# Performance work log

Hardware: AMD Instinct MI355X
Metric: run time of the kernel (lower is better)

## Reference

```python
import jax, jax.numpy as jnp
import numpy as np

N, IN_DIM, H, D = 4096, 512, 4, 64


def setup_inputs() -> dict:
    key = jax.random.key(0)
    k1, k2, k3, k4 = jax.random.split(key, 4)
    features = jax.random.normal(k1, (N, IN_DIM), dtype=jnp.float32)
    adjacency = jax.random.randint(k2, (N, N), 0, 2, dtype=jnp.int32)
    weights = jax.random.normal(k3, (IN_DIM, D * H), dtype=jnp.float32) * (1.414 / np.sqrt(IN_DIM))
    attention = jax.random.normal(k4, (1, H, 2 * D), dtype=jnp.float32) * 0.1
    bias = jnp.zeros((D * H,), dtype=jnp.float32)
    return {"features": features, "adjacency": adjacency, "weights": weights,
            "attention": attention, "bias": bias}


def reference(features, adjacency, weights, attention, bias):
    n = features.shape[0]
    h = (features @ weights).reshape(n, H, D)  # [N, H, D]
    # e[i,j,h] = leakyrelu(a1_h . h_i + a2_h . h_j)  (concat-attention decomposed)
    a1 = attention[0, :, :D]   # [H, D]
    a2 = attention[0, :, D:]   # [H, D]
    s1 = jnp.einsum('nhd,hd->nh', h, a1)  # [N, H]
    s2 = jnp.einsum('nhd,hd->nh', h, a2)  # [N, H]
    e = jax.nn.leaky_relu(s1[:, None, :] + s2[None, :, :], negative_slope=0.2)  # [N, N, H]
    masked = jnp.where(adjacency[:, :, None] > 0, e, jnp.float32(-9e15))
    attn = jax.nn.softmax(masked, axis=1)  # softmax over neighbors j (dim=1)
    out = jnp.einsum('ijh,jhd->ihd', attn, h).reshape(n, H * D)
    return out + bias
```

## Files before the change

### kernel.cpp

```cpp
#include <hip/hip_runtime.h>
#include <hip/hip_bf16.h>

#define N_NODES 4096
#define IN_DIMC 512
#define NHEADS 4
#define DHEAD 64
#define OUT_COLS 256
#define HPB (N_NODES * DHEAD * 2)

typedef __attribute__((ext_vector_type(8))) short short8;
typedef __attribute__((ext_vector_type(4))) float f32x4;

__device__ __forceinline__ short bf16b(float x) {
    return __builtin_bit_cast(short, __float2bfloat16(x));
}
__device__ __forceinline__ void gload16(const void* g, void* l) {
    __builtin_amdgcn_global_load_lds((const __attribute__((address_space(1))) void*)g,
                                     (__attribute__((address_space(3))) void*)l,
                                     16, 0, 0);
}
__device__ __forceinline__ void gload4(const void* g, void* l) {
    __builtin_amdgcn_global_load_lds((const __attribute__((address_space(1))) void*)g,
                                     (__attribute__((address_space(3))) void*)l,
                                     4, 0, 0);
}

__global__ __launch_bounds__(256) void k_prep2(
    const float* __restrict__ A, const float* __restrict__ W,
    const float* __restrict__ att, const int* __restrict__ adj,
    char* __restrict__ hP, float* __restrict__ E1, float* __restrict__ F1,
    float* __restrict__ E2, float* __restrict__ F2,
    unsigned long long* __restrict__ bitsT)
{
    const int t = (int)threadIdx.x;
    if (blockIdx.x >= 512) {
        const int pb = (int)blockIdx.x - 512;
        const int i = pb * 4 + (t >> 6);
        const int lane = t & 63;
        const int* arow = adj + (size_t)i * N_NODES;
        #pragma unroll 2
        for (int it = 0; it < 16; ++it) {
            const int c = it * 4;
            const int a0 = arow[(c + 0) * 64 + lane];
            const int a1 = arow[(c + 1) * 64 + lane];
            const int a2 = arow[(c + 2) * 64 + lane];
            const int a3 = arow[(c + 3) * 64 + lane];
            const unsigned long long m0 = __ballot(a0 != 0);
            const unsigned long long m1 = __ballot(a1 != 0);
            const unsigned long long m2 = __ballot(a2 != 0);
            const unsigned long long m3 = __ballot(a3 != 0);
            if (lane == 0) {
                bitsT[(size_t)(c + 0) * N_NODES + i] = m0;
                bitsT[(size_t)(c + 1) * N_NODES + i] = m1;
                bitsT[(size_t)(c + 2) * N_NODES + i] = m2;
                bitsT[(size_t)(c + 3) * N_NODES + i] = m3;
            }
        }
        return;
    }
    __shared__ float As[32][36];
    __shared__ float Bs[32][68];
    __shared__ float ht[64][33];
    const int m0 = ((int)blockIdx.x & 127) * 32;
    const int head = (int)blockIdx.x >> 7;
    const int n0 = head * 64;
    const int tm = t & 7, tn = t >> 3;
    float acc[4][2] = {};
    for (int k0 = 0; k0 < IN_DIMC; k0 += 32) {
        {
            const int r = t >> 3, kc = (t & 7) << 2;
            float4 v0 = *(const float4*)(A + (size_t)(m0 + r) * IN_DIMC + k0 + kc);
            As[kc + 0][r] = v0.x; As[kc + 1][r] = v0.y; As[kc + 2][r] = v0.z; As[kc + 3][r] = v0.w;
            const int rb = t >> 4, nc = (t & 15) << 2;
            float4 w0 = *(const float4*)(W + (size_t)(k0 + rb) * OUT_COLS + n0 + nc);
            float4 w1 = *(const float4*)(W + (size_t)(k0 + rb + 16) * OUT_COLS + n0 + nc);
            *(float4*)&Bs[rb][nc] = w0;
            *(float4*)&Bs[rb + 16][nc] = w1;
        }
        __syncthreads();
        #pragma unroll
        for (int kk = 0; kk < 32; ++kk) {
            const f32x4 a = *(const f32x4*)&As[kk][tm << 2];
            const float b0 = Bs[kk][tn * 2], b1 = Bs[kk][tn * 2 + 1];
            #pragma unroll
            for (int i = 0; i < 4; ++i) {
                acc[i][0] = fmaf(a[i], b0, acc[i][0]);
                acc[i][1] = fmaf(a[i], b1, acc[i][1]);
            }
        }
        __syncthreads();
    }
    #pragma unroll
    for (int i = 0; i < 4; ++i) {
        ht[tn * 2 + 0][(tm << 2) + i] = acc[i][0];
        ht[tn * 2 + 1][(tm << 2) + i] = acc[i][1];
    }
    __syncthreads();
    {
        const int d = t >> 2, qq = t & 3;
        short8 hv;
        #pragma unroll
        for (int k = 0; k < 8; ++k) hv[k] = bf16b(ht[d][qq * 8 + k]);
        const size_t off16 = ((size_t)(m0 >> 5) * 4 + (d >> 4)) * 64 + qq * 16 + (d & 15);
        *(short8*)(hP + (size_t)head * HPB + off16 * 16) = hv;
    }
    {
        const int r = t >> 3, part = t & 7;
        float p1 = 0.f, p2 = 0.f;
        #pragma unroll
        for (int dd = 0; dd < 8; ++dd) {
            const int d = part * 8 + dd;
            const float v = ht[d][r];
            p1 = fmaf(v, att[head * 128 + d], p1);
            p2 = fmaf(v, att[head * 128 + 64 + d], p2);
        }
        p1 += __shfl_xor(p1, 1); p1 += __shfl_xor(p1, 2); p1 += __shfl_xor(p1, 4);
        p2 += __shfl_xor(p2, 1); p2 += __shfl_xor(p2, 2); p2 += __shfl_xor(p2, 4);
        if (part == 0) {
            const int idx = head * N_NODES + m0 + r;
            E1[idx] = __expf(p1);
            F1[idx] = __expf(0.2f * p1);
            E2[idx] = __expf(p2);
            F2[idx] = __expf(0.2f * p2);
        }
    }
}

__global__ __launch_bounds__(512, 2) void k_gat(
    const unsigned long long* __restrict__ bitsT, const char* __restrict__ hP,
    const float* __restrict__ E1, const float* __restrict__ F1,
    const float* __restrict__ E2, const float* __restrict__ F2,
    float* __restrict__ pA, float* __restrict__ pB, float* __restrict__ pDen)
{
    __shared__ __align__(16) char stage[8 * 18432];
    const int i0 = (int)blockIdx.x * 32;
    const int by = (int)blockIdx.y;
    const int t = (int)threadIdx.x;
    const int w = t >> 6, lane = t & 63, il = lane & 15, q = lane >> 4;
    const int head = w & 3, jseg = w >> 2;
    const int jbase = by * 2048 + jseg * 1024;
    char* myst = stage + w * 18432;
    const char* hPh = hP + (size_t)head * HPB;
    const float* E2h = E2 + head * N_NODES;
    const float* F2h = F2 + head * N_NODES;
    const float e1a = E1[head * N_NODES + i0 + il];
    const float e1b = E1[head * N_NODES + i0 + 16 + il];
    const float f1a = F1[head * N_NODES + i0 + il];
    const float f1b = F1[head * N_NODES + i0 + 16 + il];
    f32x4 acc[4][2] = {};
    f32x4 accD[2] = {};
    short8 ones;
    #pragma unroll
    for (int e = 0; e < 8; ++e) ones[e] = (short)0x3F80;

    const int g0 = jbase >> 5;
    const int c0 = jbase >> 6;
    auto issue = [&](int bs, char* dst) {
        const char* hsrc = hPh + (size_t)(g0 + bs * 2) * 4096;
        #pragma unroll
        for (int k = 0; k < 8; ++k)
            gload16(hsrc + k * 1024 + lane * 16, dst + k * 1024);
        gload4(E2h + jbase + bs * 64 + lane, dst + 8192);
        gload4(F2h + jbase + bs * 64 + lane, dst + 8448);
        gload4((const char*)(bitsT + (size_t)(c0 + bs) * N_NODES + i0) + lane * 4,
               dst + 8704);
    };
    issue(0, myst);
    #pragma unroll 2
    for (int s = 0; s < 16; ++s) {
        const int bs = (s + 1 < 16) ? s + 1 : 15;
        issue(bs, myst + ((s + 1) & 1) * 9216);
        asm volatile("s_waitcnt vmcnt(11)" ::: "memory");
        const char* base = myst + (s & 1) * 9216;
        const unsigned long long bitsA = *(const unsigned long long*)(base + 8704 + il * 8);
        const unsigned long long bitsB = *(const unsigned long long*)(base + 8704 + 128 + il * 8);
        #pragma unroll
        for (int h = 0; h < 2; ++h) {
            const f32x4 ea = *(const f32x4*)(base + 8192 + h * 128 + q * 32);
            const f32x4 eb = *(const f32x4*)(base + 8192 + h * 128 + q * 32 + 16);
            const f32x4 fa = *(const f32x4*)(base + 8448 + h * 128 + q * 32);
            const f32x4 fb2 = *(const f32x4*)(base + 8448 + h * 128 + q * 32 + 16);
            const unsigned mA = (unsigned)(bitsA >> (h * 32 + q * 8)) & 0xffu;
            const unsigned mB = (unsigned)(bitsB >> (h * 32 + q * 8)) & 0xffu;
            short8 afA, afB;
            #pragma unroll
            for (int e = 0; e < 8; ++e) {
                const float Ev = (e < 4) ? ea[e] : eb[e - 4];
                const float Fv = (e < 4) ? fa[e] : fb2[e - 4];
                const float pa = fmaxf(e1a * Ev, f1a * Fv);
                const float pb = fmaxf(e1b * Ev, f1b * Fv);
                afA[e] = bf16b(((mA >> e) & 1u) ? pa : 0.f);
                afB[e] = bf16b(((mB >> e) & 1u) ? pb : 0.f);
            }
            #pragma unroll
            for (int dblk = 0; dblk < 4; ++dblk) {
                const short8 bfrag = *(const short8*)(base + h * 4096 + dblk * 1024 + lane * 16);
                acc[dblk][0] = __builtin_amdgcn_mfma_f32_16x16x32_bf16(afA, bfrag, acc[dblk][0], 0, 0, 0);
                acc[dblk][1] = __builtin_amdgcn_mfma_f32_16x16x32_bf16(afB, bfrag, acc[dblk][1], 0, 0, 0);
            }
            accD[0] = __builtin_amdgcn_mfma_f32_16x16x32_bf16(afA, ones, accD[0], 0, 0, 0);
            accD[1] = __builtin_amdgcn_mfma_f32_16x16x32_bf16(afB, ones, accD[1], 0, 0, 0);
        }
    }
    __syncthreads();
    float* ep = (float*)stage;
    if (jseg == 1) {
        float* dst = ep + (w - 4) * 2560;
        #pragma unroll
        for (int dblk = 0; dblk < 4; ++dblk)
            #pragma unroll
            for (int sub = 0; sub < 2; ++sub)
                #pragma unroll
                for (int r = 0; r < 4; ++r)
                    dst[(dblk * 8 + sub * 4 + r) * 64 + lane] = acc[dblk][sub][r];
        #pragma unroll
        for (int sub = 0; sub < 2; ++sub)
            #pragma unroll
            for (int r = 0; r < 4; ++r)
                dst[(32 + sub * 4 + r) * 64 + lane] = accD[sub][r];
    }
    __syncthreads();
    if (jseg == 0) {
        const float* src = ep + w * 2560;
        float* po = (by == 0) ? pA : pB;
        #pragma unroll
        for (int sub = 0; sub < 2; ++sub) {
            #pragma unroll
            for (int r = 0; r < 4; ++r) {
                const int row = i0 + sub * 16 + q * 4 + r;
                #pragma unroll
                for (int dblk = 0; dblk < 4; ++dblk) {
                    const float v = acc[dblk][sub][r] + src[(dblk * 8 + sub * 4 + r) * 64 + lane];
                    po[(size_t)row * OUT_COLS + head * DHEAD + dblk * 16 + il] = v;
                }
                if (il == 0) {
                    const float d = accD[sub][r] + src[(32 + sub * 4 + r) * 64 + lane];
                    pDen[by * (NHEADS * N_NODES) + head * N_NODES + row] = d;
                }
            }
        }
    }
}

__global__ __launch_bounds__(256) void k_fin(
    const float* __restrict__ pB, const float* __restrict__ pDen,
    const float* __restrict__ bias, float* __restrict__ outp)
{
    const int gid = (int)blockIdx.x * 256 + (int)threadIdx.x;
    const int i = gid >> 6;
    const int c4 = (gid & 63) << 2;
    const int head = c4 >> 6;
    const float4 v0 = *(const float4*)(outp + (size_t)i * OUT_COLS + c4);
    const float4 v1 = *(const float4*)(pB + (size_t)i * OUT_COLS + c4);
    const float d = pDen[head * N_NODES + i] + pDen[NHEADS * N_NODES + head * N_NODES + i];
    const float inv = 1.0f / d;
    const float4 bb = *(const float4*)(bias + c4);
    float4 r;
    r.x = (v0.x + v1.x) * inv + bb.x;
    r.y = (v0.y + v1.y) * inv + bb.y;
    r.z = (v0.z + v1.z) * inv + bb.z;
    r.w = (v0.w + v1.w) * inv + bb.w;
    *(float4*)(outp + (size_t)i * OUT_COLS + c4) = r;
}

extern "C" void kernel_launch(void* const* d_in, const int* in_sizes, int n_in,
                              void* d_out, int out_size, void* d_ws, size_t ws_size,
                              hipStream_t stream) {
    const float* features  = (const float*)d_in[0];
    const int*   adjacency = (const int*)d_in[1];
    const float* weights   = (const float*)d_in[2];
    const float* attention = (const float*)d_in[3];
    const float* bias      = (const float*)d_in[4];
    float* out = (float*)d_out;

    char* ws = (char*)d_ws;
    char*  hP = ws;
    float* E1 = (float*)(ws + 2u*1024*1024);
    float* F1 = (float*)(ws + 2u*1024*1024 +  64u*1024);
    float* E2 = (float*)(ws + 2u*1024*1024 + 128u*1024);
    float* F2 = (float*)(ws + 2u*1024*1024 + 192u*1024);
    unsigned long long* bitsT =
        (unsigned long long*)(ws + 2u*1024*1024 + 256u*1024);
    float* pB   = (float*)(ws + 4u*1024*1024 + 256u*1024);
    float* pDen = (float*)(ws + 8u*1024*1024 + 256u*1024);

    k_prep2<<<dim3(1536), 256, 0, stream>>>(features, weights, attention, adjacency,
                                            hP, E1, F1, E2, F2, bitsT);
    k_gat<<<dim3(128, 2), 512, 0, stream>>>(bitsT, hP, E1, F1, E2, F2,
                                            out , pB, pDen);
    k_fin<<<dim3(1024), 256, 0, stream>>>(pB, pDen, bias, out);
}
```

Measured before the change: 58.75 us.

## Split GAT neighbor loop four ways with smaller 32-column stages

The attention-aggregation kernel now splits the neighbor dimension four ways instead of two, launching 512 blocks instead of 256. Each wave processes 32 neighbors per step with a halved LDS stage, and launch bounds are raised to four blocks per SM. The adjacency bitmask is stored as 32-bit words so each step can load only the bits it needs. The aim is more parallelism and occupancy on the main kernel, at the cost of two extra partial-output buffers that the final kernel must read and sum, and a shorter pipeline per block.

Measured after the change: 60.74 us. 3.4% more time.

```diff
diff --git a/kernel.cpp b/kernel.cpp
--- a/kernel.cpp
+++ b/kernel.cpp
@@ -30,7 +30,7 @@
     const float* __restrict__ att, const int* __restrict__ adj,
     char* __restrict__ hP, float* __restrict__ E1, float* __restrict__ F1,
     float* __restrict__ E2, float* __restrict__ F2,
-    unsigned long long* __restrict__ bitsT)
+    unsigned* __restrict__ bits32)
 {
     const int t = (int)threadIdx.x;
     if (blockIdx.x >= 512) {
@@ -50,10 +50,14 @@
             const unsigned long long m2 = __ballot(a2 != 0);
             const unsigned long long m3 = __ballot(a3 != 0);
             if (lane == 0) {
-                bitsT[(size_t)(c + 0) * N_NODES + i] = m0;
-                bitsT[(size_t)(c + 1) * N_NODES + i] = m1;
-                bitsT[(size_t)(c + 2) * N_NODES + i] = m2;
-                bitsT[(size_t)(c + 3) * N_NODES + i] = m3;
+                bits32[(size_t)(2 * c + 0) * N_NODES + i] = (unsigned)m0;
+                bits32[(size_t)(2 * c + 1) * N_NODES + i] = (unsigned)(m0 >> 32);
+                bits32[(size_t)(2 * c + 2) * N_NODES + i] = (unsigned)m1;
+                bits32[(size_t)(2 * c + 3) * N_NODES + i] = (unsigned)(m1 >> 32);
+                bits32[(size_t)(2 * c + 4) * N_NODES + i] = (unsigned)m2;
+                bits32[(size_t)(2 * c + 5) * N_NODES + i] = (unsigned)(m2 >> 32);
+                bits32[(size_t)(2 * c + 6) * N_NODES + i] = (unsigned)m3;
+                bits32[(size_t)(2 * c + 7) * N_NODES + i] = (unsigned)(m3 >> 32);
             }
         }
         return;
@@ -126,20 +130,21 @@
     }
 }
 
-__global__ __launch_bounds__(512, 2) void k_gat(
-    const unsigned long long* __restrict__ bitsT, const char* __restrict__ hP,
+__global__ __launch_bounds__(512, 4) void k_gat(
+    const unsigned* __restrict__ bits32, const char* __restrict__ hP,
     const float* __restrict__ E1, const float* __restrict__ F1,
     const float* __restrict__ E2, const float* __restrict__ F2,
-    float* __restrict__ pA, float* __restrict__ pB, float* __restrict__ pDen)
+    float* __restrict__ pA, float* __restrict__ pB,
+    float* __restrict__ pC, float* __restrict__ pD, float* __restrict__ pDen)
 {
-    __shared__ __align__(16) char stage[8 * 18432];
+    __shared__ __align__(16) char stage[8 * 9216];
     const int i0 = (int)blockIdx.x * 32;
     const int by = (int)blockIdx.y;
     const int t = (int)threadIdx.x;
     const int w = t >> 6, lane = t & 63, il = lane & 15, q = lane >> 4;
     const int head = w & 3, jseg = w >> 2;
-    const int jbase = by * 2048 + jseg * 1024;
-    char* myst = stage + w * 18432;
+    const int jbase = by * 1024 + jseg * 512;
+    char* myst = stage + w * 9216;
     const char* hPh = hP + (size_t)head * HPB;
     const float* E2h = E2 + head * N_NODES;
     const float* F2h = F2 + head * N_NODES;
@@ -154,53 +159,54 @@
     for (int e = 0; e < 8; ++e) ones[e] = (short)0x3F80;
 
     const int g0 = jbase >> 5;
-    const int c0 = jbase >> 6;
     auto issue = [&](int bs, char* dst) {
-        const char* hsrc = hPh + (size_t)(g0 + bs * 2) * 4096;
-        #pragma unroll
-        for (int k = 0; k < 8; ++k)
+        const char* hsrc = hPh + (size_t)(g0 + bs) * 4096;
+        #pragma unroll
+        for (int k = 0; k < 4; ++k)
             gload16(hsrc + k * 1024 + lane * 16, dst + k * 1024);
-        gload4(E2h + jbase + bs * 64 + lane, dst + 8192);
-        gload4(F2h + jbase + bs * 64 + lane, dst + 8448);
-        gload4((const char*)(bitsT + (size_t)(c0 + bs) * N_NODES + i0) + lane * 4,
-               dst + 8704);
+        if (lane < 32) {
+            gload4(E2h + jbase + bs * 32 + lane, dst + 4096);
+            gload4(F2h + jbase + bs * 32 + lane, dst + 4224);
+            gload4((const char*)(bits32 + (size_t)(g0 + bs) * N_NODES + i0) + lane * 4,
+                   dst + 4352);
+        }
     };
     issue(0, myst);
     #pragma unroll 2
     for (int s = 0; s < 16; ++s) {
-        const int bs = (s + 1 < 16) ? s + 1 : 15;
-        issue(bs, myst + ((s + 1) & 1) * 9216);
-        asm volatile("s_waitcnt vmcnt(11)" ::: "memory");
-        const char* base = myst + (s & 1) * 9216;
-        const unsigned long long bitsA = *(const unsigned long long*)(base + 8704 + il * 8);
-        const unsigned long long bitsB = *(const unsigned long long*)(base + 8704 + 128 + il * 8);
-        #pragma unroll
-        for (int h = 0; h < 2; ++h) {
-            const f32x4 ea = *(const f32x4*)(base + 8192 + h * 128 + q * 32);
-            const f32x4 eb = *(const f32x4*)(base + 8192 + h * 128 + q * 32 + 16);
-            const f32x4 fa = *(const f32x4*)(base + 8448 + h * 128 + q * 32);
-            const f32x4 fb2 = *(const f32x4*)(base + 8448 + h * 128 + q * 32 + 16);
-            const unsigned mA = (unsigned)(bitsA >> (h * 32 + q * 8)) & 0xffu;
-            const unsigned mB = (unsigned)(bitsB >> (h * 32 + q * 8)) & 0xffu;
-            short8 afA, afB;
-            #pragma unroll
-            for (int e = 0; e < 8; ++e) {
-                const float Ev = (e < 4) ? ea[e] : eb[e - 4];
-                const float Fv = (e < 4) ? fa[e] : fb2[e - 4];
-                const float pa = fmaxf(e1a * Ev, f1a * Fv);
-                const float pb = fmaxf(e1b * Ev, f1b * Fv);
-                afA[e] = bf16b(((mA >> e) & 1u) ? pa : 0.f);
-                afB[e] = bf16b(((mB >> e) & 1u) ? pb : 0.f);
-            }
-            #pragma unroll
-            for (int dblk = 0; dblk < 4; ++dblk) {
-                const short8 bfrag = *(const short8*)(base + h * 4096 + dblk * 1024 + lane * 16);
-                acc[dblk][0] = __builtin_amdgcn_mfma_f32_16x16x32_bf16(afA, bfrag, acc[dblk][0], 0, 0, 0);
-                acc[dblk][1] = __builtin_amdgcn_mfma_f32_16x16x32_bf16(afB, bfrag, acc[dblk][1], 0, 0, 0);
-            }
-            accD[0] = __builtin_amdgcn_mfma_f32_16x16x32_bf16(afA, ones, accD[0], 0, 0, 0);
-            accD[1] = __builtin_amdgcn_mfma_f32_16x16x32_bf16(afB, ones, accD[1], 0, 0, 0);
-        }
+        if (s < 15) {
+            issue(s + 1, myst + ((s + 1) & 1) * 4608);
+            asm volatile("s_waitcnt vmcnt(7)" ::: "memory");
+        } else {
+            asm volatile("s_waitcnt vmcnt(0)" ::: "memory");
+        }
+        const char* base = myst + (s & 1) * 4608;
+        const unsigned uA = *(const unsigned*)(base + 4352 + il * 4);
+        const unsigned uB = *(const unsigned*)(base + 4352 + 64 + il * 4);
+        const f32x4 ea = *(const f32x4*)(base + 4096 + q * 32);
+        const f32x4 eb = *(const f32x4*)(base + 4096 + q * 32 + 16);
+        const f32x4 fa = *(const f32x4*)(base + 4224 + q * 32);
+        const f32x4 fb2 = *(const f32x4*)(base + 4224 + q * 32 + 16);
+        const unsigned mA = (uA >> (q * 8)) & 0xffu;
+        const unsigned mB = (uB >> (q * 8)) & 0xffu;
+        short8 afA, afB;
+        #pragma unroll
+        for (int e = 0; e < 8; ++e) {
+            const float Ev = (e < 4) ? ea[e] : eb[e - 4];
+            const float Fv = (e < 4) ? fa[e] : fb2[e - 4];
+            const float pa = fmaxf(e1a * Ev, f1a * Fv);
+            const float pb = fmaxf(e1b * Ev, f1b * Fv);
+            afA[e] = bf16b(((mA >> e) & 1u) ? pa : 0.f);
+            afB[e] = bf16b(((mB >> e) & 1u) ? pb : 0.f);
+        }
+        #pragma unroll
+        for (int dblk = 0; dblk < 4; ++dblk) {
+            const short8 bfrag = *(const short8*)(base + dblk * 1024 + lane * 16);
+            acc[dblk][0] = __builtin_amdgcn_mfma_f32_16x16x32_bf16(afA, bfrag, acc[dblk][0], 0, 0, 0);
+            acc[dblk][1] = __builtin_amdgcn_mfma_f32_16x16x32_bf16(afB, bfrag, acc[dblk][1], 0, 0, 0);
+        }
+        accD[0] = __builtin_amdgcn_mfma_f32_16x16x32_bf16(afA, ones, accD[0], 0, 0, 0);
+        accD[1] = __builtin_amdgcn_mfma_f32_16x16x32_bf16(afB, ones, accD[1], 0, 0, 0);
     }
     __syncthreads();
     float* ep = (float*)stage;
@@ -222,7 +228,7 @@
     __syncthreads();
     if (jseg == 0) {
         const float* src = ep + w * 2560;
-        float* po = (by == 0) ? pA : pB;
+        float* po = (by == 0) ? pA : (by == 1) ? pB : (by == 2) ? pC : pD;
         #pragma unroll
         for (int sub = 0; sub < 2; ++sub) {
             #pragma unroll
@@ -243,7 +249,8 @@
 }
 
 __global__ __launch_bounds__(256) void k_fin(
-    const float* __restrict__ pB, const float* __restrict__ pDen,
+    const float* __restrict__ pB, const float* __restrict__ pC,
+    const float* __restrict__ pD, const float* __restrict__ pDen,
     const float* __restrict__ bias, float* __restrict__ outp)
 {
     const int gid = (int)blockIdx.x * 256 + (int)threadIdx.x;
@@ -252,14 +259,19 @@
     const int head = c4 >> 6;
     const float4 v0 = *(const float4*)(outp + (size_t)i * OUT_COLS + c4);
     const float4 v1 = *(const float4*)(pB + (size_t)i * OUT_COLS + c4);
-    const float d = pDen[head * N_NODES + i] + pDen[NHEADS * N_NODES + head * N_NODES + i];
+    const float4 v2 = *(const float4*)(pC + (size_t)i * OUT_COLS + c4);
+    const float4 v3 = *(const float4*)(pD + (size_t)i * OUT_COLS + c4);
+    const float d = pDen[head * N_NODES + i]
+                  + pDen[1 * NHEADS * N_NODES + head * N_NODES + i]
+                  + pDen[2 * NHEADS * N_NODES + head * N_NODES + i]
+                  + pDen[3 * NHEADS * N_NODES + head * N_NODES + i];
     const float inv = 1.0f / d;
     const float4 bb = *(const float4*)(bias + c4);
     float4 r;
-    r.x = (v0.x + v1.x) * inv + bb.x;
-    r.y = (v0.y + v1.y) * inv + bb.y;
-    r.z = (v0.z + v1.z) * inv + bb.z;
-    r.w = (v0.w + v1.w) * inv + bb.w;
+    r.x = (v0.x + v1.x + v2.x + v3.x) * inv + bb.x;
+    r.y = (v0.y + v1.y + v2.y + v3.y) * inv + bb.y;
+    r.z = (v0.z + v1.z + v2.z + v3.z) * inv + bb.z;
+    r.w = (v0.w + v1.w + v2.w + v3.w) * inv + bb.w;
     *(float4*)(outp + (size_t)i * OUT_COLS + c4) = r;
 }
 
@@ -274,19 +286,20 @@
     float* out = (float*)d_out;
 
     char* ws = (char*)d_ws;
-    char*  hP = ws;
-    float* E1 = (float*)(ws + 2u*1024*1024);
-    float* F1 = (float*)(ws + 2u*1024*1024 +  64u*1024);
-    float* E2 = (float*)(ws + 2u*1024*1024 + 128u*1024);
-    float* F2 = (float*)(ws + 2u*1024*1024 + 192u*1024);
-    unsigned long long* bitsT =
-        (unsigned long long*)(ws + 2u*1024*1024 + 256u*1024);
-    float* pB   = (float*)(ws + 4u*1024*1024 + 256u*1024);
-    float* pDen = (float*)(ws + 8u*1024*1024 + 256u*1024);
+    char*     hP     = ws;
+    float*    E1     = (float*)(ws + 2u*1024*1024);
+    float*    F1     = (float*)(ws + 2u*1024*1024 +  64u*1024);
+    float*    E2     = (float*)(ws + 2u*1024*1024 + 128u*1024);
+    float*    F2     = (float*)(ws + 2u*1024*1024 + 192u*1024);
+    unsigned* bits32 = (unsigned*)(ws + 2u*1024*1024 + 256u*1024);
+    float*    pB     = (float*)(ws + 4u*1024*1024 + 256u*1024);
+    float*    pC     = (float*)(ws + 8u*1024*1024 + 256u*1024);
+    float*    pD     = (float*)(ws + 12u*1024*1024 + 256u*1024);
+    float*    pDen   = (float*)(ws + 16u*1024*1024 + 256u*1024);
 
     k_prep2<<<dim3(1536), 256, 0, stream>>>(features, weights, attention, adjacency,
-                                            hP, E1, F1, E2, F2, bitsT);
-    k_gat<<<dim3(128, 2), 512, 0, stream>>>(bitsT, hP, E1, F1, E2, F2,
-                                            out , pB, pDen);
-    k_fin<<<dim3(1024), 256, 0, stream>>>(pB, pDen, bias, out);
-}
+                                            hP, E1, F1, E2, F2, bits32);
+    k_gat<<<dim3(128, 4), 512, 0, stream>>>(bits32, hP, E1, F1, E2, F2,
+                                            out , pB, pC, pD, pDen);
+    k_fin<<<dim3(1024), 256, 0, stream>>>(pB, pC, pD, pDen, bias, out);
+}
```

## Stage adjacency bitmask transpose in LDS for coalesced stores; skip redundant final prefetch

Applied to the files above, without the earlier changes.

Each adjacency-packing block now handles 32 rows instead of 4. Its ballot bitmasks are staged in shared memory and then written to the transposed bitsT layout as 32 consecutive 8-byte words per column. Before, each row's masks were scattered single 8-byte stores. The grid shrinks from 1536 to 640 blocks, and the gat loop no longer reissues a redundant prefetch on its last iteration. Fewer packing blocks means less parallelism for streaming the 64MB adjacency matrix.

After: 91.29 us. +55.4%, slower.

```diff
diff --git a/kernel.cpp b/kernel.cpp
--- a/kernel.cpp
+++ b/kernel.cpp
@@ -34,27 +34,40 @@
 {
     const int t = (int)threadIdx.x;
     if (blockIdx.x >= 512) {
+        __shared__ unsigned ldsbits[32][130];
         const int pb = (int)blockIdx.x - 512;
-        const int i = pb * 4 + (t >> 6);
-        const int lane = t & 63;
-        const int* arow = adj + (size_t)i * N_NODES;
+        const int i0p = pb * 32;
+        const int w = t >> 6, lane = t & 63;
         #pragma unroll 2
-        for (int it = 0; it < 16; ++it) {
-            const int c = it * 4;
-            const int a0 = arow[(c + 0) * 64 + lane];
-            const int a1 = arow[(c + 1) * 64 + lane];
-            const int a2 = arow[(c + 2) * 64 + lane];
-            const int a3 = arow[(c + 3) * 64 + lane];
-            const unsigned long long m0 = __ballot(a0 != 0);
-            const unsigned long long m1 = __ballot(a1 != 0);
-            const unsigned long long m2 = __ballot(a2 != 0);
-            const unsigned long long m3 = __ballot(a3 != 0);
-            if (lane == 0) {
-                bitsT[(size_t)(c + 0) * N_NODES + i] = m0;
-                bitsT[(size_t)(c + 1) * N_NODES + i] = m1;
-                bitsT[(size_t)(c + 2) * N_NODES + i] = m2;
-                bitsT[(size_t)(c + 3) * N_NODES + i] = m3;
-            }
+        for (int rr = 0; rr < 8; ++rr) {
+            const int rl = (w << 3) | rr;
+            const int* arow = adj + (size_t)(i0p + rl) * N_NODES;
+            for (int cb = 0; cb < 16; ++cb) {
+                const int c = cb * 4;
+                const int a0 = arow[(c + 0) * 64 + lane];
+                const int a1 = arow[(c + 1) * 64 + lane];
+                const int a2 = arow[(c + 2) * 64 + lane];
+                const int a3 = arow[(c + 3) * 64 + lane];
+                const unsigned long long m0 = __ballot(a0 != 0);
+                const unsigned long long m1 = __ballot(a1 != 0);
+                const unsigned long long m2 = __ballot(a2 != 0);
+                const unsigned long long m3 = __ballot(a3 != 0);
+                if (lane == 0) {
+                    *(unsigned long long*)&ldsbits[rl][(c + 0) * 2] = m0;
+                    *(unsigned long long*)&ldsbits[rl][(c + 1) * 2] = m1;
+                    *(unsigned long long*)&ldsbits[rl][(c + 2) * 2] = m2;
+                    *(unsigned long long*)&ldsbits[rl][(c + 3) * 2] = m3;
+                }
+            }
+        }
+        __syncthreads();
+        #pragma unroll
+        for (int it = 0; it < 8; ++it) {
+            const int c = (w << 4) + it * 2 + (lane >> 5);
+            const int r = lane & 31;
+            const unsigned long long v =
+                *(const unsigned long long*)&ldsbits[r][c * 2];
+            bitsT[(size_t)c * N_NODES + i0p + r] = v;
         }
         return;
     }
@@ -168,9 +181,12 @@
     issue(0, myst);
     #pragma unroll 2
     for (int s = 0; s < 16; ++s) {
-        const int bs = (s + 1 < 16) ? s + 1 : 15;
-        issue(bs, myst + ((s + 1) & 1) * 9216);
-        asm volatile("s_waitcnt vmcnt(11)" ::: "memory");
+        if (s < 15) {
+            issue(s + 1, myst + ((s + 1) & 1) * 9216);
+            asm volatile("s_waitcnt vmcnt(11)" ::: "memory");
+        } else {
+            asm volatile("s_waitcnt vmcnt(0)" ::: "memory");
+        }
         const char* base = myst + (s & 1) * 9216;
         const unsigned long long bitsA = *(const unsigned long long*)(base + 8704 + il * 8);
         const unsigned long long bitsB = *(const unsigned long long*)(base + 8704 + 128 + il * 8);
@@ -284,8 +300,8 @@
     float* pB   = (float*)(ws + 4u*1024*1024 + 256u*1024);
     float* pDen = (float*)(ws + 8u*1024*1024 + 256u*1024);
 
-    k_prep2<<<dim3(1536), 256, 0, stream>>>(features, weights, attention, adjacency,
-                                            hP, E1, F1, E2, F2, bitsT);
+    k_prep2<<<dim3(640), 256, 0, stream>>>(features, weights, attention, adjacency,
+                                           hP, E1, F1, E2, F2, bitsT);
     k_gat<<<dim3(128, 2), 512, 0, stream>>>(bitsT, hP, E1, F1, E2, F2,
                                             out , pB, pDen);
     k_fin<<<dim3(1024), 256, 0, stream>>>(pB, pDen, bias, out);
```

## Read adjacency as int4 and repack bitmask, E2/F2, h into permuted layouts

Applied to the files above, without the earlier changes.

The adjacency bitmask pass now reads int4 per lane, which is fully coalesced 16-byte loads instead of strided scalar loads. It packs ballots into 32-bit words in a permuted column order, and E2/F2 and the bf16 h layout are permuted to match. The attention kernel reads 32-bit mask words per row and drops the redundant final prefetch iteration. This relies on the column permutations being consistent across all three data streams, which adds correctness risk.

Result: slower. 60.20 us (+2.5%).

```diff
diff --git a/kernel.cpp b/kernel.cpp
--- a/kernel.cpp
+++ b/kernel.cpp
@@ -11,6 +11,7 @@
 typedef __attribute__((ext_vector_type(8))) short short8;
 typedef __attribute__((ext_vector_type(4))) float f32x4;
 
+
 __device__ __forceinline__ short bf16b(float x) {
     return __builtin_bit_cast(short, __float2bfloat16(x));
 }
@@ -29,31 +30,30 @@
     const float* __restrict__ A, const float* __restrict__ W,
     const float* __restrict__ att, const int* __restrict__ adj,
     char* __restrict__ hP, float* __restrict__ E1, float* __restrict__ F1,
-    float* __restrict__ E2, float* __restrict__ F2,
-    unsigned long long* __restrict__ bitsT)
+    float* __restrict__ E2p, float* __restrict__ F2p,
+    unsigned* __restrict__ bits32)
 {
     const int t = (int)threadIdx.x;
     if (blockIdx.x >= 512) {
         const int pb = (int)blockIdx.x - 512;
         const int i = pb * 4 + (t >> 6);
         const int lane = t & 63;
-        const int* arow = adj + (size_t)i * N_NODES;
+        const int4* arow = (const int4*)(adj + (size_t)i * N_NODES);
         #pragma unroll 2
         for (int it = 0; it < 16; ++it) {
-            const int c = it * 4;
-            const int a0 = arow[(c + 0) * 64 + lane];
-            const int a1 = arow[(c + 1) * 64 + lane];
-            const int a2 = arow[(c + 2) * 64 + lane];
-            const int a3 = arow[(c + 3) * 64 + lane];
-            const unsigned long long m0 = __ballot(a0 != 0);
-            const unsigned long long m1 = __ballot(a1 != 0);
-            const unsigned long long m2 = __ballot(a2 != 0);
-            const unsigned long long m3 = __ballot(a3 != 0);
-            if (lane == 0) {
-                bitsT[(size_t)(c + 0) * N_NODES + i] = m0;
-                bitsT[(size_t)(c + 1) * N_NODES + i] = m1;
-                bitsT[(size_t)(c + 2) * N_NODES + i] = m2;
-                bitsT[(size_t)(c + 3) * N_NODES + i] = m3;
+            const int4 a = arow[it * 64 + lane];
+            const unsigned long long m0 = __ballot(a.x != 0);
+            const unsigned long long m1 = __ballot(a.y != 0);
+            const unsigned long long m2 = __ballot(a.z != 0);
+            const unsigned long long m3 = __ballot(a.w != 0);
+            if (lane < 8) {
+                const int sh = lane * 8;
+                const unsigned wv =
+                      ((unsigned)(m0 >> sh) & 0xffu)
+                    | (((unsigned)(m1 >> sh) & 0xffu) << 8)
+                    | (((unsigned)(m2 >> sh) & 0xffu) << 16)
+                    | (((unsigned)(m3 >> sh) & 0xffu) << 24);
+                bits32[(size_t)(it * 8 + lane) * N_NODES + i] = wv;
             }
         }
         return;
@@ -100,7 +100,7 @@
         const int d = t >> 2, qq = t & 3;
         short8 hv;
         #pragma unroll
-        for (int k = 0; k < 8; ++k) hv[k] = bf16b(ht[d][qq * 8 + k]);
+        for (int e = 0; e < 8; ++e) hv[e] = bf16b(ht[d][4 * e + qq]);
         const size_t off16 = ((size_t)(m0 >> 5) * 4 + (d >> 4)) * 64 + qq * 16 + (d & 15);
         *(short8*)(hP + (size_t)head * HPB + off16 * 16) = hv;
     }
@@ -118,18 +118,19 @@
         p2 += __shfl_xor(p2, 1); p2 += __shfl_xor(p2, 2); p2 += __shfl_xor(p2, 4);
         if (part == 0) {
             const int idx = head * N_NODES + m0 + r;
+            const int idxp = head * N_NODES + m0 + ((r & 3) << 3) + (r >> 2);
             E1[idx] = __expf(p1);
             F1[idx] = __expf(0.2f * p1);
-            E2[idx] = __expf(p2);
-            F2[idx] = __expf(0.2f * p2);
+            E2p[idxp] = __expf(p2);
+            F2p[idxp] = __expf(0.2f * p2);
         }
     }
 }
 
 __global__ __launch_bounds__(512, 2) void k_gat(
-    const unsigned long long* __restrict__ bitsT, const char* __restrict__ hP,
+    const unsigned* __restrict__ bits32, const char* __restrict__ hP,
     const float* __restrict__ E1, const float* __restrict__ F1,
-    const float* __restrict__ E2, const float* __restrict__ F2,
+    const float* __restrict__ E2p, const float* __restrict__ F2p,
     float* __restrict__ pA, float* __restrict__ pB, float* __restrict__ pDen)
 {
     __shared__ __align__(16) char stage[8 * 18432];
@@ -141,8 +142,8 @@
     const int jbase = by * 2048 + jseg * 1024;
     char* myst = stage + w * 18432;
     const char* hPh = hP + (size_t)head * HPB;
-    const float* E2h = E2 + head * N_NODES;
-    const float* F2h = F2 + head * N_NODES;
+    const float* E2h = E2p + head * N_NODES;
+    const float* F2h = F2p + head * N_NODES;
     const float e1a = E1[head * N_NODES + i0 + il];
     const float e1b = E1[head * N_NODES + i0 + 16 + il];
     const float f1a = F1[head * N_NODES + i0 + il];
@@ -154,7 +155,6 @@
     for (int e = 0; e < 8; ++e) ones[e] = (short)0x3F80;
 
     const int g0 = jbase >> 5;
-    const int c0 = jbase >> 6;
     auto issue = [&](int bs, char* dst) {
         const char* hsrc = hPh + (size_t)(g0 + bs * 2) * 4096;
         #pragma unroll
@@ -162,26 +162,30 @@
             gload16(hsrc + k * 1024 + lane * 16, dst + k * 1024);
         gload4(E2h + jbase + bs * 64 + lane, dst + 8192);
         gload4(F2h + jbase + bs * 64 + lane, dst + 8448);
-        gload4((const char*)(bitsT + (size_t)(c0 + bs) * N_NODES + i0) + lane * 4,
+        gload4((const char*)bits32 +
+               ((size_t)(g0 + bs * 2 + (lane >> 5)) * N_NODES + i0 + (lane & 31)) * 4,
                dst + 8704);
     };
     issue(0, myst);
     #pragma unroll 2
     for (int s = 0; s < 16; ++s) {
-        const int bs = (s + 1 < 16) ? s + 1 : 15;
-        issue(bs, myst + ((s + 1) & 1) * 9216);
-        asm volatile("s_waitcnt vmcnt(11)" ::: "memory");
+        if (s < 15) {
+            issue(s + 1, myst + ((s + 1) & 1) * 9216);
+            asm volatile("s_waitcnt vmcnt(11)" ::: "memory");
+        } else {
+            asm volatile("s_waitcnt vmcnt(0)" ::: "memory");
+        }
         const char* base = myst + (s & 1) * 9216;
-        const unsigned long long bitsA = *(const unsigned long long*)(base + 8704 + il * 8);
-        const unsigned long long bitsB = *(const unsigned long long*)(base + 8704 + 128 + il * 8);
         #pragma unroll
         for (int h = 0; h < 2; ++h) {
             const f32x4 ea = *(const f32x4*)(base + 8192 + h * 128 + q * 32);
             const f32x4 eb = *(const f32x4*)(base + 8192 + h * 128 + q * 32 + 16);
             const f32x4 fa = *(const f32x4*)(base + 8448 + h * 128 + q * 32);
             const f32x4 fb2 = *(const f32x4*)(base + 8448 + h * 128 + q * 32 + 16);
-            const unsigned mA = (unsigned)(bitsA >> (h * 32 + q * 8)) & 0xffu;
-            const unsigned mB = (unsigned)(bitsB >> (h * 32 + q * 8)) & 0xffu;
+            const unsigned uA = *(const unsigned*)(base + 8704 + h * 128 + il * 4);
+            const unsigned uB = *(const unsigned*)(base + 8704 + h * 128 + 64 + il * 4);
+            const unsigned mA = (uA >> (q * 8)) & 0xffu;
+            const unsigned mB = (uB >> (q * 8)) & 0xffu;
             short8 afA, afB;
             #pragma unroll
             for (int e = 0; e < 8; ++e) {
@@ -274,19 +278,18 @@
     float* out = (float*)d_out;
 
     char* ws = (char*)d_ws;
-    char*  hP = ws;
-    float* E1 = (float*)(ws + 2u*1024*1024);
-    float* F1 = (float*)(ws + 2u*1024*1024 +  64u*1024);
-    float* E2 = (float*)(ws + 2u*1024*1024 + 128u*1024);
-    float* F2 = (float*)(ws + 2u*1024*1024 + 192u*1024);
-    unsigned long long* bitsT =
-        (unsigned long long*)(ws + 2u*1024*1024 + 256u*1024);
-    float* pB   = (float*)(ws + 4u*1024*1024 + 256u*1024);
-    float* pDen = (float*)(ws + 8u*1024*1024 + 256u*1024);
+    char*     hP     = ws;
+    float*    E1     = (float*)(ws + 2u*1024*1024);
+    float*    F1     = (float*)(ws + 2u*1024*1024 +  64u*1024);
+    float*    E2p    = (float*)(ws + 2u*1024*1024 + 128u*1024);
+    float*    F2p    = (float*)(ws + 2u*1024*1024 + 192u*1024);
+    unsigned* bits32 = (unsigned*)(ws + 2u*1024*1024 + 256u*1024);
+    float*    pB     = (float*)(ws + 4u*1024*1024 + 256u*1024);
+    float*    pDen   = (float*)(ws + 8u*1024*1024 + 256u*1024);
 
     k_prep2<<<dim3(1536), 256, 0, stream>>>(features, weights, attention, adjacency,
-                                            hP, E1, F1, E2, F2, bitsT);
-    k_gat<<<dim3(128, 2), 512, 0, stream>>>(bitsT, hP, E1, F1, E2, F2,
+                                            hP, E1, F1, E2p, F2p, bits32);
+    k_gat<<<dim3(128, 2), 512, 0, stream>>>(bits32, hP, E1, F1, E2p, F2p,
                                             out , pB, pDen);
     k_fin<<<dim3(1024), 256, 0, stream>>>(pB, pDen, bias, out);
 }
```
